# Kernel tuning notes

Hardware: AMD Instinct MI355X
Metric: run time of the kernel (lower is better)

## Reference

```python
import jax, jax.numpy as jnp
import numpy as np

H, T, E = 8, 2048, 512


def setup_inputs() -> dict:
    key = jax.random.key(0)
    ks = jax.random.split(key, 11)
    s_e = 1.0 / np.sqrt(E)
    s_f = 1.0 / np.sqrt(H * T)
    return {
        "x": jax.random.normal(ks[0], (T, E), jnp.float32),
        "y": jax.random.normal(ks[1], (T, E), jnp.float32),
        "z": jax.random.normal(ks[2], (T, E), jnp.float32),
        "Wq": jax.random.normal(ks[3], (H, E, E), jnp.float32) * s_e,
        "bq": jax.random.normal(ks[4], (H, E), jnp.float32) * s_e,
        "Wk": jax.random.normal(ks[5], (H, E, E), jnp.float32) * s_e,
        "bk": jax.random.normal(ks[6], (H, E), jnp.float32) * s_e,
        "Wv": jax.random.normal(ks[7], (H, E, E), jnp.float32) * s_e,
        "bv": jax.random.normal(ks[8], (H, E), jnp.float32) * s_e,
        "Wf": jax.random.normal(ks[9], (T, H * T), jnp.float32) * s_f,
        "bf": jax.random.normal(ks[10], (T,), jnp.float32) * s_f,
    }


def reference(x, y, z, Wq, bq, Wk, bk, Wv, bv, Wf, bf):
    # Per-head projections: torch Linear is x @ W.T + b, W is [out,in]
    q = jnp.einsum("se,hfe->hsf", x, Wq) + bq[:, None, :]  # [H,T,E]
    k = jnp.einsum("se,hfe->hsf", y, Wk) + bk[:, None, :]
    v = jnp.einsum("se,hfe->hsf", z, Wv) + bv[:, None, :]
    # Scores scaled by sqrt(num query rows) = sqrt(T), as in the source
    scores = jnp.einsum("hsf,htf->hst", q, k) / jnp.sqrt(jnp.asarray(T, x.dtype))
    att = jax.nn.softmax(scores, axis=-1)
    heads_out = jnp.einsum("hst,htf->hsf", att, v)  # [H,T,E]
    concat = heads_out.reshape(H * T, E)  # cat along dim 0
    # finalLinear applied to concat.T: [E, H*T] @ Wf.T -> [E, T], then transpose
    final = (concat.T @ Wf.T + bf).T  # [T, E]
    residual = final + z
    # Manual per-row LayerNorm: (x - mean) / sqrt(std^2 + 1e-4), population std
    mean = jnp.mean(residual, axis=1, keepdims=True)
    var = jnp.var(residual, axis=1, keepdims=True)
    return (residual - mean) / jnp.sqrt(var + 1e-4)
```

## Files before the change

kernel.cpp:

```cpp
#include <hip/hip_runtime.h>
#include <hip/hip_bf16.h>
#include <cstdint>


#define HH 8
#define TT 2048
#define EE 512
#define HT (HH * TT)
#define HE (HH * EE)

typedef __bf16 bf16_t;
typedef __attribute__((ext_vector_type(8))) __bf16 bf16x8;
typedef __attribute__((ext_vector_type(4))) float f32x4;

__device__ __forceinline__ void gld_lds16(const bf16_t* __restrict__ g, bf16_t* l) {
  __builtin_amdgcn_global_load_lds(
      (const __attribute__((address_space(1))) unsigned int*)g,
      (__attribute__((address_space(3))) unsigned int*)l, 16, 0, 0);
}

__device__ __forceinline__ bf16x8 cvt8(float4 u, float4 v) {
  bf16x8 o;
  o[0] = (__bf16)u.x; o[1] = (__bf16)u.y; o[2] = (__bf16)u.z; o[3] = (__bf16)u.w;
  o[4] = (__bf16)v.x; o[5] = (__bf16)v.y; o[6] = (__bf16)v.z; o[7] = (__bf16)v.w;
  return o;
}

#define XCD_SWIZZLE()                                                              \
  const int gx = gridDim.x, gy = gridDim.y;                                        \
  const int nwg = gx * gy * (int)gridDim.z;                                        \
  const int lin = blockIdx.x + gx * (blockIdx.y + gy * blockIdx.z);                \
  const int qn_ = nwg >> 3, rn_ = nwg & 7;                                         \
  const int xcd_ = lin & 7, sub_ = lin >> 3;                                       \
  const int wgid =                                                                 \
      (xcd_ < rn_ ? xcd_ * (qn_ + 1) : rn_ * (qn_ + 1) + (xcd_ - rn_) * qn_) + sub_; \
  const int bx = wgid % gx;                                                        \
  const int t1_ = wgid / gx;                                                       \
  const int by = t1_ % gy;                                                         \
  const int z = t1_ / gy;

template <typename CT>
__global__ __launch_bounds__(512, 2) void gemm256_8ph(
    const bf16_t* __restrict__ A, const bf16_t* __restrict__ B, CT* __restrict__ C,
    const float* __restrict__ bias_n,
    int K, int lda, int ldb, int ldc,
    int64_t sA, int64_t sB, int64_t sC, int64_t sBN) {
  XCD_SWIZZLE();
  A += z * sA;
  B += z * sB;
  C += z * sC;
  if (bias_n) bias_n += z * sBN;

  const int m0 = bx * 256;
  const int n0 = by * 256;
  const int tid = threadIdx.x;

  __shared__ bf16_t lds[65536];
  bf16_t* sAl = lds;
  bf16_t* sBl = lds + 32768;

  const int srow = tid >> 3;
  const int csw = ((tid & 7) ^ (srow & 7)) * 8;
  const bf16_t* aS = A + (int64_t)(m0 + srow) * lda + csw;
  const bf16_t* bS = B + (int64_t)(n0 + srow) * ldb + csw;
  const int64_t l64a = (int64_t)64 * lda, l64b = (int64_t)64 * ldb;

  const int wave = tid >> 6, lane = tid & 63;
  const int wr = wave >> 2, wc = wave & 3;
  const int fr = lane & 15, qd = lane >> 4;
  const int aoff = wr * 8192 + fr * 64;
  const int boff = wc * 4096 + fr * 64;
  const int ck0 = ((0 * 4 + qd) ^ (fr & 7)) * 8;
  const int ck1 = ((1 * 4 + qd) ^ (fr & 7)) * 8;

  f32x4 acc[8][4];
#pragma unroll
  for (int i = 0; i < 8; i++)
#pragma unroll
    for (int j = 0; j < 4; j++) acc[i][j] = (f32x4){0.f, 0.f, 0.f, 0.f};

  bf16x8 aR[2][8];
  bf16x8 bR[2][2];

#define STG_A(d, h, t)                                                        \
  do {                                                                        \
    const bf16_t* g_ = aS + (int64_t)(h) * 128 * lda + (int64_t)(t) * 64;     \
    gld_lds16(g_, &sAl[(d) * 16384 + (h) * 8192 + tid * 8]);                  \
    gld_lds16(g_ + l64a, &sAl[(d) * 16384 + (h) * 8192 + 4096 + tid * 8]);    \
  } while (0)
#define STG_B(d, h, t)                                                        \
  do {                                                                        \
    const bf16_t* g_ = bS + (int64_t)(h) * 128 * ldb + (int64_t)(t) * 64;     \
    gld_lds16(g_, &sBl[(d) * 16384 + (h) * 8192 + tid * 8]);                  \
    gld_lds16(g_ + l64b, &sBl[(d) * 16384 + (h) * 8192 + 4096 + tid * 8]);    \
  } while (0)
#define RD_A(d, ih)                                                           \
  _Pragma("unroll") for (int i_ = 0; i_ < 4; i_++) {                          \
    const int b_ = (d) * 16384 + aoff + ((ih) * 4 + i_) * 1024;               \
    aR[0][(ih) * 4 + i_] = *(const bf16x8*)&sAl[b_ + ck0];                    \
    aR[1][(ih) * 4 + i_] = *(const bf16x8*)&sAl[b_ + ck1];                    \
  }
#define RD_B(d, jh)                                                           \
  _Pragma("unroll") for (int j_ = 0; j_ < 2; j_++) {                          \
    const int b_ = (d) * 16384 + boff + ((jh) * 2 + j_) * 1024;               \
    bR[0][j_] = *(const bf16x8*)&sBl[b_ + ck0];                               \
    bR[1][j_] = *(const bf16x8*)&sBl[b_ + ck1];                               \
  }
#define MM(qm, qn)                                                            \
  do {                                                                        \
    __builtin_amdgcn_s_setprio(1);                                            \
    _Pragma("unroll") for (int ks = 0; ks < 2; ks++)                          \
        _Pragma("unroll") for (int i_ = 0; i_ < 4; i_++)                      \
            _Pragma("unroll") for (int j_ = 0; j_ < 2; j_++)                  \
                acc[(qm) * 4 + i_][(qn) * 2 + j_] =                           \
                    __builtin_amdgcn_mfma_f32_16x16x32_bf16(                  \
                        aR[ks][(qm) * 4 + i_], bR[ks][j_],                    \
                        acc[(qm) * 4 + i_][(qn) * 2 + j_], 0, 0, 0);          \
    __builtin_amdgcn_s_setprio(0);                                            \
  } while (0)
#define BAR __builtin_amdgcn_s_barrier()
#define LGKM0                                                                 \
  do {                                                                        \
    asm volatile("s_waitcnt lgkmcnt(0)" ::: "memory");                        \
    __builtin_amdgcn_sched_barrier(0);                                        \
  } while (0)
#define VMC(n)                                                                \
  do {                                                                        \
    asm volatile("s_waitcnt vmcnt(" #n ")" ::: "memory");                     \
    __builtin_amdgcn_sched_barrier(0);                                        \
  } while (0)

  const int NT = K >> 6;

  STG_A(0, 0, 0); STG_A(0, 1, 0); STG_B(0, 0, 0); STG_B(0, 1, 0);
  STG_A(1, 0, 1); STG_A(1, 1, 1);
  VMC(4);
  BAR;

  for (int t0 = 0; t0 < NT; t0 += 2) {
    const int t1 = t0 + 1;
    const bool m2 = (t0 + 2) < NT;
    RD_A(0, 0); RD_B(0, 0);
    STG_B(1, 0, t1);
    BAR; LGKM0; MM(0, 0); BAR;
    RD_A(0, 1);
    STG_B(1, 1, t1);
    BAR; LGKM0; MM(1, 0); BAR;
    RD_B(0, 1);
    if (m2) STG_A(0, 0, t0 + 2);
    BAR; LGKM0; MM(0, 1); BAR;
    if (m2) STG_A(0, 1, t0 + 2);
    BAR; MM(1, 1);
    if (m2) { VMC(4); } else { VMC(0); }
    BAR;
    RD_A(1, 0); RD_B(1, 0);
    if (m2) STG_B(0, 0, t0 + 2);
    BAR; LGKM0; MM(0, 0); BAR;
    RD_A(1, 1);
    if (m2) STG_B(0, 1, t0 + 2);
    BAR; LGKM0; MM(1, 0); BAR;
    RD_B(1, 1);
    if (m2) STG_A(1, 0, t1 + 2);
    BAR; LGKM0; MM(0, 1); BAR;
    if (m2) STG_A(1, 1, t1 + 2);
    BAR; MM(1, 1);
    if (m2) VMC(4);
    BAR;
  }

#undef STG_A
#undef STG_B
#undef RD_A
#undef RD_B
#undef MM
#undef BAR
#undef LGKM0
#undef VMC

#pragma unroll
  for (int i = 0; i < 8; i++) {
    const int row0 = m0 + wr * 128 + i * 16 + qd * 4;
#pragma unroll
    for (int j = 0; j < 4; j++) {
      const int col = n0 + wc * 64 + j * 16 + fr;
      const float bn = bias_n ? bias_n[col] : 0.f;
#pragma unroll
      for (int r = 0; r < 4; r++)
        C[(int64_t)(row0 + r) * ldc + col] = (CT)(acc[i][j][r] + bn);
    }
  }
}

template <typename AT, typename CT>
__global__ __launch_bounds__(512, 4) void mfma_gemm_nt(
    const AT* __restrict__ A, const bf16_t* __restrict__ B, CT* __restrict__ C,
    const float* __restrict__ bias_m, const float* __restrict__ bias_n,
    int K, int lda, int ldb, int ldc,
    int64_t sA, int64_t sB, int64_t sC, int64_t sBM, int64_t sBN) {
  XCD_SWIZZLE();
  A += z * sA;
  B += z * sB;
  C += z * sC;
  if (bias_m) bias_m += z * sBM;
  if (bias_n) bias_n += z * sBN;

  const int m0 = bx * 128;
  const int n0 = by * 128;
  const int tid = threadIdx.x;

  __shared__ bf16_t sAb[2][128 * 64];
  __shared__ bf16_t sBb[2][128 * 64];

  const int srow = tid >> 3;
  const int sc = tid & 7;
  const int csw = (sc ^ (srow & 7)) * 8;
  const AT* a0 = A + (int64_t)(m0 + srow) * lda + csw;
  const AT* a1 = a0 + (int64_t)64 * lda;
  const bf16_t* b0 = B + (int64_t)(n0 + srow) * ldb + csw;
  const bf16_t* b1 = b0 + (int64_t)64 * ldb;

  const int wave = tid >> 6;
  const int lane = tid & 63;
  const int wm = (wave >> 2) * 64;
  const int wn = (wave & 3) * 32;
  const int fr = lane & 15;
  const int qd = lane >> 4;
  const int cx0 = ((0 * 4 + qd) ^ (fr & 7)) * 8;
  const int cx1 = ((1 * 4 + qd) ^ (fr & 7)) * 8;

  f32x4 acc[4][2];
#pragma unroll
  for (int i = 0; i < 4; i++)
#pragma unroll
    for (int j = 0; j < 2; j++) acc[i][j] = (f32x4){0.f, 0.f, 0.f, 0.f};

  float4 pa[4];

#define STAGE_B(buf, kt)                              \
  do {                                                \
    gld_lds16(b0 + (kt), &sBb[buf][tid * 8]);         \
    gld_lds16(b1 + (kt), &sBb[buf][4096 + tid * 8]);  \
  } while (0)
#define STAGE_A_BF16(buf, kt)                         \
  do {                                                \
    gld_lds16(a0 + (kt), &sAb[buf][tid * 8]);         \
    gld_lds16(a1 + (kt), &sAb[buf][4096 + tid * 8]);  \
  } while (0)
#define LOAD_A_F32(kt)                                \
  do {                                                \
    pa[0] = ((const float4*)(a0 + (kt)))[0];          \
    pa[1] = ((const float4*)(a0 + (kt)))[1];          \
    pa[2] = ((const float4*)(a1 + (kt)))[0];          \
    pa[3] = ((const float4*)(a1 + (kt)))[1];          \
  } while (0)
#define WRITE_A_F32(buf)                                      \
  do {                                                        \
    *(bf16x8*)&sAb[buf][tid * 8] = cvt8(pa[0], pa[1]);        \
    *(bf16x8*)&sAb[buf][4096 + tid * 8] = cvt8(pa[2], pa[3]); \
  } while (0)
#define COMPUTE(buf)                                                                   \
  do {                                                                                 \
    bf16x8 af[2][4], bfr[2][2];                                                        \
    _Pragma("unroll") for (int i = 0; i < 4; i++) {                                    \
      const int ar = (wm + i * 16 + fr) * 64;                                          \
      af[0][i] = *(const bf16x8*)&sAb[buf][ar + cx0];                                  \
      af[1][i] = *(const bf16x8*)&sAb[buf][ar + cx1];                                  \
    }                                                                                  \
    _Pragma("unroll") for (int j = 0; j < 2; j++) {                                    \
      const int br = (wn + j * 16 + fr) * 64;                                          \
      bfr[0][j] = *(const bf16x8*)&sBb[buf][br + cx0];                                 \
      bfr[1][j] = *(const bf16x8*)&sBb[buf][br + cx1];                                 \
    }                                                                                  \
    _Pragma("unroll") for (int ks = 0; ks < 2; ks++)                                   \
        _Pragma("unroll") for (int i = 0; i < 4; i++)                                  \
            _Pragma("unroll") for (int j = 0; j < 2; j++)                              \
                acc[i][j] = __builtin_amdgcn_mfma_f32_16x16x32_bf16(                   \
                    af[ks][i], bfr[ks][j], acc[i][j], 0, 0, 0);                        \
  } while (0)

  if constexpr (sizeof(AT) == 2) {
    STAGE_A_BF16(0, 0);
  } else {
    LOAD_A_F32(0);
    WRITE_A_F32(0);
  }
  STAGE_B(0, 0);
  __syncthreads();

  for (int kt = 0; kt < K; kt += 128) {
    if constexpr (sizeof(AT) == 2) {
      STAGE_A_BF16(1, kt + 64);
    } else {
      LOAD_A_F32(kt + 64);
    }
    STAGE_B(1, kt + 64);
    COMPUTE(0);
    if constexpr (sizeof(AT) == 4) WRITE_A_F32(1);
    __syncthreads();

    const bool more = (kt + 128) < K;
    if (more) {
      if constexpr (sizeof(AT) == 2) {
        STAGE_A_BF16(0, kt + 128);
      } else {
        LOAD_A_F32(kt + 128);
      }
      STAGE_B(0, kt + 128);
    }
    COMPUTE(1);
    if constexpr (sizeof(AT) == 4) {
      if (more) WRITE_A_F32(0);
    }
    __syncthreads();
  }

#undef STAGE_B
#undef STAGE_A_BF16
#undef LOAD_A_F32
#undef WRITE_A_F32
#undef COMPUTE

#pragma unroll
  for (int i = 0; i < 4; i++) {
    const int row0 = m0 + wm + i * 16 + qd * 4;
#pragma unroll
    for (int j = 0; j < 2; j++) {
      const int col = n0 + wn + j * 16 + fr;
      const float bn = bias_n ? bias_n[col] : 0.f;
#pragma unroll
      for (int r = 0; r < 4; r++) {
        const float bm = bias_m ? bias_m[row0 + r] : 0.f;
        C[(int64_t)(row0 + r) * ldc + col] = (CT)(acc[i][j][r] + bn + bm);
      }
    }
  }
}

__global__ __launch_bounds__(256) void cvt_bf16(const float* __restrict__ s,
                                                bf16_t* __restrict__ d) {
  const int64_t i = ((int64_t)blockIdx.x * 256 + threadIdx.x) * 8;
  float4 u = ((const float4*)(s + i))[0];
  float4 v = ((const float4*)(s + i))[1];
  *(bf16x8*)(d + i) = cvt8(u, v);
}

__global__ __launch_bounds__(256) void softmax_rows(bf16_t* __restrict__ S) {
  const float scale = 0.022097086912079608f;
  bf16_t* p = S + (int64_t)blockIdx.x * TT;
  const int tid = threadIdx.x;
  bf16x8 in = *(const bf16x8*)(p + tid * 8);
  float v[8];
  float mx = -1e30f;
#pragma unroll
  for (int i = 0; i < 8; i++) {
    v[i] = (float)in[i] * scale;
    mx = fmaxf(mx, v[i]);
  }
#pragma unroll
  for (int o = 32; o > 0; o >>= 1) mx = fmaxf(mx, __shfl_xor(mx, o));
  __shared__ float redm[4], reds[4];
  if ((tid & 63) == 0) redm[tid >> 6] = mx;
  __syncthreads();
  mx = fmaxf(fmaxf(redm[0], redm[1]), fmaxf(redm[2], redm[3]));
  float sum = 0.f;
#pragma unroll
  for (int i = 0; i < 8; i++) {
    v[i] = __expf(v[i] - mx);
    sum += v[i];
  }
#pragma unroll
  for (int o = 32; o > 0; o >>= 1) sum += __shfl_xor(sum, o);
  if ((tid & 63) == 0) reds[tid >> 6] = sum;
  __syncthreads();
  sum = reds[0] + reds[1] + reds[2] + reds[3];
  const float inv = 1.0f / sum;
  bf16x8 o8;
#pragma unroll
  for (int i = 0; i < 8; i++) o8[i] = (__bf16)(v[i] * inv);
  *(bf16x8*)(p + tid * 8) = o8;
}

__global__ __launch_bounds__(256) void ln_res(const float* __restrict__ F,
                                              const float* __restrict__ Z,
                                              const float* __restrict__ BF,
                                              float* __restrict__ O, int np) {
  const int row = blockIdx.x;
  const int tid = threadIdx.x;
  const int64_t off = (int64_t)row * EE + tid;
  float a = 0.f, b = 0.f;
  for (int pz = 0; pz < np; pz++) {
    const float* f = F + (int64_t)pz * TT * EE;
    a += f[off];
    b += f[off + 256];
  }
  const float bft = BF[row];
  a += bft + Z[off];
  b += bft + Z[off + 256];
  float s = a + b, ss = a * a + b * b;
#pragma unroll
  for (int w = 32; w > 0; w >>= 1) {
    s += __shfl_xor(s, w);
    ss += __shfl_xor(ss, w);
  }
  __shared__ float rs[4], rss[4];
  if ((tid & 63) == 0) {
    rs[tid >> 6] = s;
    rss[tid >> 6] = ss;
  }
  __syncthreads();
  s = rs[0] + rs[1] + rs[2] + rs[3];
  ss = rss[0] + rss[1] + rss[2] + rss[3];
  const float mean = s * (1.0f / EE);
  const float var = ss * (1.0f / EE) - mean * mean;
  const float inv = rsqrtf(var + 1e-4f);
  float* o = O + (int64_t)row * EE;
  o[tid] = (a - mean) * inv;
  o[tid + 256] = (b - mean) * inv;
}

extern "C" void kernel_launch(void* const* d_in, const int* in_sizes, int n_in,
                              void* d_out, int out_size, void* d_ws, size_t ws_size,
                              hipStream_t stream) {
  const float* x = (const float*)d_in[0];
  const float* y = (const float*)d_in[1];
  const float* z = (const float*)d_in[2];
  const float* Wq = (const float*)d_in[3];
  const float* bq = (const float*)d_in[4];
  const float* Wk = (const float*)d_in[5];
  const float* bk = (const float*)d_in[6];
  const float* Wv = (const float*)d_in[7];
  const float* bv = (const float*)d_in[8];
  const float* Wf = (const float*)d_in[9];
  const float* bfb = (const float*)d_in[10];
  float* out = (float*)d_out;

  const size_t MB = 1ull << 20;
  char* p = (char*)d_ws;

  const int64_t nTE = (int64_t)TT * EE;
  const int64_t nW = (int64_t)HH * EE * EE;

  if (ws_size >= 151 * MB) {
    bf16_t* xb = (bf16_t*)(p + 0 * MB);
    bf16_t* yb = (bf16_t*)(p + 2 * MB);
    bf16_t* zb = (bf16_t*)(p + 4 * MB);
    bf16_t* Wqb = (bf16_t*)(p + 6 * MB);
    bf16_t* Wkb = (bf16_t*)(p + 10 * MB);
    bf16_t* Wvb = (bf16_t*)(p + 14 * MB);
    bf16_t* q = (bf16_t*)(p + 18 * MB);
    bf16_t* k = (bf16_t*)(p + 34 * MB);
    bf16_t* vT = (bf16_t*)(p + 50 * MB);
    bf16_t* att = (bf16_t*)(p + 66 * MB);
    bf16_t* hoT = (bf16_t*)(p + 130 * MB);
    float* finp = (float*)(p + 66 * MB);
    float* bqk = (float*)(p + 146 * MB);

    cvt_bf16<<<nTE / 2048, 256, 0, stream>>>(x, xb);
    cvt_bf16<<<nTE / 2048, 256, 0, stream>>>(y, yb);
    cvt_bf16<<<nTE / 2048, 256, 0, stream>>>(z, zb);
    cvt_bf16<<<nW / 2048, 256, 0, stream>>>(Wq, Wqb);
    cvt_bf16<<<nW / 2048, 256, 0, stream>>>(Wk, Wkb);
    cvt_bf16<<<nW / 2048, 256, 0, stream>>>(Wv, Wvb);
    hipMemcpyAsync(bqk, bq, HE * sizeof(float), hipMemcpyDeviceToDevice, stream);
    hipMemcpyAsync(bqk + HE, bk, HE * sizeof(float), hipMemcpyDeviceToDevice, stream);

    gemm256_8ph<bf16_t><<<dim3(8, 16, 2), 512, 0, stream>>>(
        xb, Wqb, q, bqk, EE, EE, EE, HE,
        (int64_t)TT * EE, (int64_t)HE * EE, (int64_t)TT * HE, HE);
    mfma_gemm_nt<bf16_t, bf16_t><<<dim3(32, 16, 1), 512, 0, stream>>>(
        Wvb, zb, vT, bv, nullptr, EE, EE, EE, TT, 0, 0, 0, 0, 0);
    gemm256_8ph<bf16_t><<<dim3(8, 8, 8), 512, 0, stream>>>(
        q, k, att, nullptr, EE, HE, HE, TT, EE, EE, (int64_t)TT * TT, 0);
    softmax_rows<<<HH * TT, 256, 0, stream>>>(att);
    mfma_gemm_nt<bf16_t, bf16_t><<<dim3(4, 16, 8), 512, 0, stream>>>(
        vT, att, hoT, nullptr, nullptr, TT, TT, TT, HT, (int64_t)EE * TT, (int64_t)TT * TT,
        (int64_t)TT, 0, 0);
    mfma_gemm_nt<float, float><<<dim3(16, 4, 8), 512, 0, stream>>>(
        Wf, hoT, finp, nullptr, nullptr, HT / 8, HT, HT, EE, HT / 8, HT / 8,
        (int64_t)TT * EE, 0, 0);
    ln_res<<<TT, 256, 0, stream>>>(finp, z, bfb, out, 8);
  } else {
    bf16_t* xb = (bf16_t*)(p + 0 * MB);
    bf16_t* yb = (bf16_t*)(p + 2 * MB);
    bf16_t* zb = (bf16_t*)(p + 4 * MB);
    bf16_t* Wqb = (bf16_t*)(p + 6 * MB);
    bf16_t* Wkb = (bf16_t*)(p + 10 * MB);
    bf16_t* Wvb = (bf16_t*)(p + 14 * MB);
    bf16_t* qh = (bf16_t*)(p + 18 * MB);
    bf16_t* kh = (bf16_t*)(p + 20 * MB);
    bf16_t* vTh = (bf16_t*)(p + 22 * MB);
    bf16_t* att = (bf16_t*)(p + 24 * MB);
    bf16_t* hoT = (bf16_t*)(p + 32 * MB);
    float* finp = (float*)(p + 0 * MB);

    cvt_bf16<<<nTE / 2048, 256, 0, stream>>>(x, xb);
    cvt_bf16<<<nTE / 2048, 256, 0, stream>>>(y, yb);
    cvt_bf16<<<nTE / 2048, 256, 0, stream>>>(z, zb);
    cvt_bf16<<<nW / 2048, 256, 0, stream>>>(Wq, Wqb);
    cvt_bf16<<<nW / 2048, 256, 0, stream>>>(Wk, Wkb);
    cvt_bf16<<<nW / 2048, 256, 0, stream>>>(Wv, Wvb);

    for (int h = 0; h < HH; h++) {
      const bf16_t* Wq_h = Wqb + (int64_t)h * EE * EE;
      const bf16_t* Wk_h = Wkb + (int64_t)h * EE * EE;
      const bf16_t* Wv_h = Wvb + (int64_t)h * EE * EE;
      mfma_gemm_nt<bf16_t, bf16_t><<<dim3(16, 4, 1), 512, 0, stream>>>(
          xb, Wq_h, qh, nullptr, bq + h * EE, EE, EE, EE, EE, 0, 0, 0, 0, 0);
      mfma_gemm_nt<bf16_t, bf16_t><<<dim3(16, 4, 1), 512, 0, stream>>>(
          yb, Wk_h, kh, nullptr, bk + h * EE, EE, EE, EE, EE, 0, 0, 0, 0, 0);
      mfma_gemm_nt<bf16_t, bf16_t><<<dim3(4, 16, 1), 512, 0, stream>>>(
          Wv_h, zb, vTh, bv + h * EE, nullptr, EE, EE, EE, TT, 0, 0, 0, 0, 0);
      mfma_gemm_nt<bf16_t, bf16_t><<<dim3(16, 16, 1), 512, 0, stream>>>(
          qh, kh, att, nullptr, nullptr, EE, EE, EE, TT, 0, 0, 0, 0, 0);
      softmax_rows<<<TT, 256, 0, stream>>>(att);
      mfma_gemm_nt<bf16_t, bf16_t><<<dim3(4, 16, 1), 512, 0, stream>>>(
          vTh, att, hoT + (int64_t)h * TT, nullptr, nullptr, TT, TT, TT, HT, 0, 0, 0, 0, 0);
    }
    mfma_gemm_nt<float, float><<<dim3(16, 4, 8), 512, 0, stream>>>(
        Wf, hoT, finp, nullptr, nullptr, HT / 8, HT, HT, EE, HT / 8, HT / 8,
        (int64_t)TT * EE, 0, 0);
    ln_res<<<TT, 256, 0, stream>>>(finp, z, bfb, out, 8);
  }
}
```

Measured before the change: 428.8 us.

## Fuse six bf16 conversion kernels into one and split Q/K projection launches

Replaces six separate fp32-to-bf16 conversion launches with one kernel that picks its source tensor from the block index, removing launch overhead and tail gaps between small kernels. It also drops the bias-concatenation memcpys and the batched 256-tile Q/K projection kernel, using two mfma_gemm_nt launches (one for Q, one for K) with a row bias instead. The generic GEMM may be less efficient than the specialised 256-tile kernel for the projections.

```diff
diff --git a/kernel.cpp b/kernel.cpp
--- a/kernel.cpp
+++ b/kernel.cpp
@@ -336,9 +336,23 @@
   }
 }
 
-__global__ __launch_bounds__(256) void cvt_bf16(const float* __restrict__ s,
-                                                bf16_t* __restrict__ d) {
-  const int64_t i = ((int64_t)blockIdx.x * 256 + threadIdx.x) * 8;
+__global__ __launch_bounds__(256) void fused_cvt(
+    const float* __restrict__ x, const float* __restrict__ y,
+    const float* __restrict__ z, const float* __restrict__ Wq,
+    const float* __restrict__ Wk, const float* __restrict__ Wv,
+    bf16_t* __restrict__ xb, bf16_t* __restrict__ yb, bf16_t* __restrict__ zb,
+    bf16_t* __restrict__ Wqb, bf16_t* __restrict__ Wkb, bf16_t* __restrict__ Wvb) {
+  const int b = blockIdx.x;
+  const float* s;
+  bf16_t* d;
+  int off;
+  if (b < 512) { s = x; d = xb; off = b; }
+  else if (b < 1024) { s = y; d = yb; off = b - 512; }
+  else if (b < 1536) { s = z; d = zb; off = b - 1024; }
+  else if (b < 2560) { s = Wq; d = Wqb; off = b - 1536; }
+  else if (b < 3584) { s = Wk; d = Wkb; off = b - 2560; }
+  else { s = Wv; d = Wvb; off = b - 3584; }
+  const int64_t i = ((int64_t)off * 256 + threadIdx.x) * 8;
   float4 u = ((const float4*)(s + i))[0];
   float4 v = ((const float4*)(s + i))[1];
   *(bf16x8*)(d + i) = cvt8(u, v);
@@ -437,9 +451,6 @@
   const size_t MB = 1ull << 20;
   char* p = (char*)d_ws;
 
-  const int64_t nTE = (int64_t)TT * EE;
-  const int64_t nW = (int64_t)HH * EE * EE;
-
   if (ws_size >= 151 * MB) {
     bf16_t* xb = (bf16_t*)(p + 0 * MB);
     bf16_t* yb = (bf16_t*)(p + 2 * MB);
@@ -453,20 +464,13 @@
     bf16_t* att = (bf16_t*)(p + 66 * MB);
     bf16_t* hoT = (bf16_t*)(p + 130 * MB);
     float* finp = (float*)(p + 66 * MB);
-    float* bqk = (float*)(p + 146 * MB);
-
-    cvt_bf16<<<nTE / 2048, 256, 0, stream>>>(x, xb);
-    cvt_bf16<<<nTE / 2048, 256, 0, stream>>>(y, yb);
-    cvt_bf16<<<nTE / 2048, 256, 0, stream>>>(z, zb);
-    cvt_bf16<<<nW / 2048, 256, 0, stream>>>(Wq, Wqb);
-    cvt_bf16<<<nW / 2048, 256, 0, stream>>>(Wk, Wkb);
-    cvt_bf16<<<nW / 2048, 256, 0, stream>>>(Wv, Wvb);
-    hipMemcpyAsync(bqk, bq, HE * sizeof(float), hipMemcpyDeviceToDevice, stream);
-    hipMemcpyAsync(bqk + HE, bk, HE * sizeof(float), hipMemcpyDeviceToDevice, stream);
-
-    gemm256_8ph<bf16_t><<<dim3(8, 16, 2), 512, 0, stream>>>(
-        xb, Wqb, q, bqk, EE, EE, EE, HE,
-        (int64_t)TT * EE, (int64_t)HE * EE, (int64_t)TT * HE, HE);
+
+    fused_cvt<<<4608, 256, 0, stream>>>(x, y, z, Wq, Wk, Wv, xb, yb, zb, Wqb, Wkb, Wvb);
+
+    mfma_gemm_nt<bf16_t, bf16_t><<<dim3(16, 32, 1), 512, 0, stream>>>(
+        xb, Wqb, q, nullptr, bq, EE, EE, EE, HE, 0, 0, 0, 0, 0);
+    mfma_gemm_nt<bf16_t, bf16_t><<<dim3(16, 32, 1), 512, 0, stream>>>(
+        yb, Wkb, k, nullptr, bk, EE, EE, EE, HE, 0, 0, 0, 0, 0);
     mfma_gemm_nt<bf16_t, bf16_t><<<dim3(32, 16, 1), 512, 0, stream>>>(
         Wvb, zb, vT, bv, nullptr, EE, EE, EE, TT, 0, 0, 0, 0, 0);
     gemm256_8ph<bf16_t><<<dim3(8, 8, 8), 512, 0, stream>>>(
@@ -493,12 +497,7 @@
     bf16_t* hoT = (bf16_t*)(p + 32 * MB);
     float* finp = (float*)(p + 0 * MB);
 
-    cvt_bf16<<<nTE / 2048, 256, 0, stream>>>(x, xb);
-    cvt_bf16<<<nTE / 2048, 256, 0, stream>>>(y, yb);
-    cvt_bf16<<<nTE / 2048, 256, 0, stream>>>(z, zb);
-    cvt_bf16<<<nW / 2048, 256, 0, stream>>>(Wq, Wqb);
-    cvt_bf16<<<nW / 2048, 256, 0, stream>>>(Wk, Wkb);
-    cvt_bf16<<<nW / 2048, 256, 0, stream>>>(Wv, Wvb);
+    fused_cvt<<<4608, 256, 0, stream>>>(x, y, z, Wq, Wk, Wv, xb, yb, zb, Wqb, Wkb, Wvb);
 
     for (int h = 0; h < HH; h++) {
       const bf16_t* Wq_h = Wqb + (int64_t)h * EE * EE;
```

Result: no change. 428.3 us (-0.1%).
